# Kernel optimization log

Measured on AMD Instinct MI355X. Metric: run time of the kernel, lower is better.

Reference implementation:

```python
import jax, jax.numpy as jnp
import numpy as np

B, L, D, U = 4, 1024, 64, 32

def setup_inputs() -> dict:
    key = jax.random.key(0)
    ks = jax.random.split(key, 6)
    inputs = jax.random.normal(ks[0], (B, L, D), dtype=jnp.float32)
    Wt = jax.random.normal(ks[1], (D, U), dtype=jnp.float32) * 0.1
    Wx = jax.random.normal(ks[2], (D, U), dtype=jnp.float32) * 0.1
    Wa = jax.random.normal(ks[3], (U, 1), dtype=jnp.float32) * 0.1
    bh = jax.random.normal(ks[4], (U,), dtype=jnp.float32) * 0.1
    ba = jax.random.normal(ks[5], (1,), dtype=jnp.float32) * 0.1
    return {"inputs": inputs, "Wt": Wt, "Wx": Wx, "Wa": Wa,
            "bh": bh, "ba": ba, "attention_width": 0}

def reference(inputs, Wt, Wx, Wa, bh, ba, attention_width):
    # Additive (Bahdanau) self-attention emission.
    q = inputs @ Wt                              # (B, L, U)
    k = inputs @ Wx                              # (B, L, U)
    # broadcast add -> (B, L, L, U), the dominant intermediate
    h = jnp.tanh(q[:, :, None, :] + k[:, None, :, :] + bh)
    e = jnp.squeeze(h @ Wa, axis=-1) + ba        # (B, L, L); ba broadcasts
    # NOTE: attention_width mask is dead code in the original forward -> ignored.
    # manual max-subtracted softmax with +1e-8 denominator (as in source)
    m = jnp.max(e, axis=-1, keepdims=True)
    ex = jnp.exp(e - m)
    a = ex / (jnp.sum(ex, axis=-1, keepdims=True) + 1e-8)
    v = jnp.einsum('bij,bjd->bid', a, inputs)    # (B, L, D)
    return v
```

## Files before the change

### kernel.cpp

```cpp
#include <hip/hip_runtime.h>

#define BB 4
#define LL 1024
#define DD 64
#define UU 32
#define TI 8
#define NT 512

__global__ __launch_bounds__(256) void precompute_kernel(
    const float* __restrict__ inp, const float* __restrict__ Wt,
    const float* __restrict__ Wx, const float* __restrict__ bh,
    float* __restrict__ Eq, float* __restrict__ Ekt)
{
    __shared__ float s_in[8][DD];
    __shared__ float s_wt[DD][UU];
    __shared__ float s_wx[DD][UU];
    __shared__ float s_ek[8][36];
    int t = threadIdx.x;
    int row0 = blockIdx.x * 8;
    if (t < 128)
        ((float4*)s_in)[t] = ((const float4*)(inp + (size_t)row0 * DD))[t];
#pragma unroll
    for (int p = 0; p < 2; ++p) {
        ((float4*)s_wt)[p * 256 + t] = ((const float4*)Wt)[p * 256 + t];
        ((float4*)s_wx)[p * 256 + t] = ((const float4*)Wx)[p * 256 + t];
    }
    __syncthreads();
    int r = t >> 5;
    int u = t & 31;
    size_t row = row0 + r;
    float q = 0.f, k = 0.f;
#pragma unroll
    for (int d = 0; d < DD; ++d) {
        float x = s_in[r][d];
        q = fmaf(x, s_wt[d][u], q);
        k = fmaf(x, s_wx[d][u], k);
    }
    Eq[row * UU + u] = __expf(2.f * (q + bh[u]));
    s_ek[r][u] = __expf(2.f * k);
    __syncthreads();
    if (t < 64) {
        int u4 = t >> 3, r2 = t & 7;
        float4 v = *(const float4*)(&s_ek[r2][u4 * 4]);
        size_t gr = row0 + r2;
        size_t bb_ = gr >> 10, l = gr & 1023;
        ((float4*)Ekt)[(bb_ * 8 + u4) * LL + l] = v;
    }
}

union ShMem {
    struct { float a0[LL][4]; float a1[LL][4]; } a;
    float4 v[8][TI][16];
};

__global__ __launch_bounds__(NT) void attn_kernel(
    const float* __restrict__ Eq, const float* __restrict__ Ekt,
    const float* __restrict__ inp, const float* __restrict__ Wa,
    float* __restrict__ out)
{
    __shared__ ShMem sh;
    __shared__ float s_red[2][8][TI];

    int t  = threadIdx.x;
    int w  = t >> 6;
    int b  = blockIdx.x >> 7;
    int i0 = (blockIdx.x & 127) * TI;

    const float4* ektb = (const float4*)Ekt + (size_t)b * 8 * LL;
    const float*  eqb  = Eq + ((size_t)(b * LL + i0)) * UU;

    float acc[TI][2];
#pragma unroll
    for (int i = 0; i < TI; ++i) { acc[i][0] = 0.f; acc[i][1] = 0.f; }

    float4 cur0 = ektb[t], cur1 = ektb[NT + t];

#pragma unroll
    for (int u4 = 0; u4 < 8; ++u4) {
        float4 nxt0, nxt1;
        if (u4 < 7) {
            nxt0 = ektb[(u4 + 1) * LL + t];
            nxt1 = ektb[(u4 + 1) * LL + NT + t];
        }
        const float* waq = Wa + u4 * 4;
        float wa0 = waq[0], wa1 = waq[1], wa2 = waq[2], wa3 = waq[3];
#pragma unroll
        for (int i = 0; i < TI; ++i) {
            const float* eqq = eqb + i * UU + u4 * 4;
            float eq0 = eqq[0], eq1 = eqq[1], eq2 = eqq[2], eq3 = eqq[3];
#pragma unroll
            for (int jj = 0; jj < 2; ++jj) {
                float4 ek = jj ? cur1 : cur0;
                float p  = fmaf(eq0, ek.x, 1.f);
                float q  = fmaf(eq1, ek.y, 1.f);
                float r  = fmaf(eq2, ek.z, 1.f);
                float s  = fmaf(eq3, ek.w, 1.f);
                float n01 = fmaf(wa0, q, wa1 * p);
                float n23 = fmaf(wa2, s, wa3 * r);
                float pq = p * q, rs = r * s;
                float num = fmaf(n01, rs, n23 * pq);
                float den = pq * rs;
                acc[i][jj] = fmaf(num, __builtin_amdgcn_rcpf(den), acc[i][jj]);
            }
        }
        if (u4 < 7) { cur0 = nxt0; cur1 = nxt1; }
    }

    float ev[TI][2];
#pragma unroll
    for (int i = 0; i < TI; ++i) {
        ev[i][0] = -2.f * acc[i][0];
        ev[i][1] = -2.f * acc[i][1];
    }

    float wred[TI];
#pragma unroll
    for (int i = 0; i < TI; ++i) {
        float v = fmaxf(ev[i][0], ev[i][1]);
#pragma unroll
        for (int m = 32; m >= 1; m >>= 1) v = fmaxf(v, __shfl_xor(v, m, 64));
        wred[i] = v;
    }
    if ((t & 63) == 0) {
#pragma unroll
        for (int i = 0; i < TI; ++i) s_red[0][w][i] = wred[i];
    }
    __syncthreads();
    float m[TI];
#pragma unroll
    for (int i = 0; i < TI; ++i) {
        float v = s_red[0][0][i];
#pragma unroll
        for (int w2 = 1; w2 < 8; ++w2) v = fmaxf(v, s_red[0][w2][i]);
        m[i] = v;
    }

#pragma unroll
    for (int i = 0; i < TI; ++i) {
        ev[i][0] = __expf(ev[i][0] - m[i]);
        ev[i][1] = __expf(ev[i][1] - m[i]);
        float s = ev[i][0] + ev[i][1];
#pragma unroll
        for (int mm = 32; mm >= 1; mm >>= 1) s += __shfl_xor(s, mm, 64);
        wred[i] = s;
    }
    if ((t & 63) == 0) {
#pragma unroll
        for (int i = 0; i < TI; ++i) s_red[1][w][i] = wred[i];
    }
    __syncthreads();
    float rs[TI];
#pragma unroll
    for (int i = 0; i < TI; ++i) {
        float s = 0.f;
#pragma unroll
        for (int w2 = 0; w2 < 8; ++w2) s += s_red[1][w2][i];
        rs[i] = 1.0f / (s + 1e-8f);
    }

#pragma unroll
    for (int jj = 0; jj < 2; ++jj) {
        int j = jj * NT + t;
        float4 lo, hi;
        lo.x = ev[0][jj] * rs[0]; lo.y = ev[1][jj] * rs[1];
        lo.z = ev[2][jj] * rs[2]; lo.w = ev[3][jj] * rs[3];
        hi.x = ev[4][jj] * rs[4]; hi.y = ev[5][jj] * rs[5];
        hi.z = ev[6][jj] * rs[6]; hi.w = ev[7][jj] * rs[7];
        *(float4*)(&sh.a.a0[j][0]) = lo;
        *(float4*)(&sh.a.a1[j][0]) = hi;
    }
    __syncthreads();

    int dq = t & 15;
    int g  = t >> 4;
    const float4* inp4 = (const float4*)(inp + (size_t)b * LL * DD);
    float4 v[TI];
#pragma unroll
    for (int i = 0; i < TI; ++i) v[i] = (float4){0.f, 0.f, 0.f, 0.f};

#pragma unroll 4
    for (int jj = 0; jj < 32; ++jj) {
        int j = jj * 32 + g;
        float4 x  = inp4[j * 16 + dq];
        float4 a0 = *(const float4*)(&sh.a.a0[j][0]);
        float4 a1 = *(const float4*)(&sh.a.a1[j][0]);
        v[0].x = fmaf(a0.x, x.x, v[0].x); v[0].y = fmaf(a0.x, x.y, v[0].y);
        v[0].z = fmaf(a0.x, x.z, v[0].z); v[0].w = fmaf(a0.x, x.w, v[0].w);
        v[1].x = fmaf(a0.y, x.x, v[1].x); v[1].y = fmaf(a0.y, x.y, v[1].y);
        v[1].z = fmaf(a0.y, x.z, v[1].z); v[1].w = fmaf(a0.y, x.w, v[1].w);
        v[2].x = fmaf(a0.z, x.x, v[2].x); v[2].y = fmaf(a0.z, x.y, v[2].y);
        v[2].z = fmaf(a0.z, x.z, v[2].z); v[2].w = fmaf(a0.z, x.w, v[2].w);
        v[3].x = fmaf(a0.w, x.x, v[3].x); v[3].y = fmaf(a0.w, x.y, v[3].y);
        v[3].z = fmaf(a0.w, x.z, v[3].z); v[3].w = fmaf(a0.w, x.w, v[3].w);
        v[4].x = fmaf(a1.x, x.x, v[4].x); v[4].y = fmaf(a1.x, x.y, v[4].y);
        v[4].z = fmaf(a1.x, x.z, v[4].z); v[4].w = fmaf(a1.x, x.w, v[4].w);
        v[5].x = fmaf(a1.y, x.x, v[5].x); v[5].y = fmaf(a1.y, x.y, v[5].y);
        v[5].z = fmaf(a1.y, x.z, v[5].z); v[5].w = fmaf(a1.y, x.w, v[5].w);
        v[6].x = fmaf(a1.z, x.x, v[6].x); v[6].y = fmaf(a1.z, x.y, v[6].y);
        v[6].z = fmaf(a1.z, x.z, v[6].z); v[6].w = fmaf(a1.z, x.w, v[6].w);
        v[7].x = fmaf(a1.w, x.x, v[7].x); v[7].y = fmaf(a1.w, x.y, v[7].y);
        v[7].z = fmaf(a1.w, x.z, v[7].z); v[7].w = fmaf(a1.w, x.w, v[7].w);
    }

#pragma unroll
    for (int i = 0; i < TI; ++i) {
        v[i].x += __shfl_xor(v[i].x, 16, 64); v[i].y += __shfl_xor(v[i].y, 16, 64);
        v[i].z += __shfl_xor(v[i].z, 16, 64); v[i].w += __shfl_xor(v[i].w, 16, 64);
        v[i].x += __shfl_xor(v[i].x, 32, 64); v[i].y += __shfl_xor(v[i].y, 32, 64);
        v[i].z += __shfl_xor(v[i].z, 32, 64); v[i].w += __shfl_xor(v[i].w, 32, 64);
    }
    __syncthreads();
    if ((t & 63) < 16) {
#pragma unroll
        for (int i = 0; i < TI; ++i) sh.v[w][i][dq] = v[i];
    }
    __syncthreads();

    int i = t >> 6;
    int d = t & 63;
    const float* svf = (const float*)sh.v;
    float r = 0.f;
#pragma unroll
    for (int w2 = 0; w2 < 8; ++w2) r += svf[w2 * (TI * 64) + i * 64 + d];
    out[((size_t)b * LL + (i0 + i)) * DD + d] = r;
}

extern "C" void kernel_launch(void* const* d_in, const int* in_sizes, int n_in,
                              void* d_out, int out_size, void* d_ws, size_t ws_size,
                              hipStream_t stream) {
    const float* inp = (const float*)d_in[0];
    const float* Wt  = (const float*)d_in[1];
    const float* Wx  = (const float*)d_in[2];
    const float* Wa  = (const float*)d_in[3];
    const float* bh  = (const float*)d_in[4];
    float* out = (float*)d_out;

    float* Eq  = (float*)d_ws;
    float* Ekt = Eq + (size_t)BB * LL * UU;

    precompute_kernel<<<BB * LL / 8, 256, 0, stream>>>(inp, Wt, Wx, bh, Eq, Ekt);
    attn_kernel<<<BB * LL / TI, NT, 0, stream>>>(Eq, Ekt, inp, Wa, out);
}
```

Measured before the change: 98.20 us.

## Fuse query projection into attention kernel and prefetch input rows

```diff
diff --git a/kernel.cpp b/kernel.cpp
--- a/kernel.cpp
+++ b/kernel.cpp
@@ -8,12 +8,10 @@
 #define NT 512
 
 __global__ __launch_bounds__(256) void precompute_kernel(
-    const float* __restrict__ inp, const float* __restrict__ Wt,
-    const float* __restrict__ Wx, const float* __restrict__ bh,
-    float* __restrict__ Eq, float* __restrict__ Ekt)
+    const float* __restrict__ inp, const float* __restrict__ Wx,
+    float* __restrict__ Ekt)
 {
     __shared__ float s_in[8][DD];
-    __shared__ float s_wt[DD][UU];
     __shared__ float s_wx[DD][UU];
     __shared__ float s_ek[8][36];
     int t = threadIdx.x;
@@ -21,22 +19,15 @@
     if (t < 128)
         ((float4*)s_in)[t] = ((const float4*)(inp + (size_t)row0 * DD))[t];
 #pragma unroll
-    for (int p = 0; p < 2; ++p) {
-        ((float4*)s_wt)[p * 256 + t] = ((const float4*)Wt)[p * 256 + t];
+    for (int p = 0; p < 2; ++p)
         ((float4*)s_wx)[p * 256 + t] = ((const float4*)Wx)[p * 256 + t];
-    }
     __syncthreads();
     int r = t >> 5;
     int u = t & 31;
-    size_t row = row0 + r;
-    float q = 0.f, k = 0.f;
-#pragma unroll
-    for (int d = 0; d < DD; ++d) {
-        float x = s_in[r][d];
-        q = fmaf(x, s_wt[d][u], q);
-        k = fmaf(x, s_wx[d][u], k);
-    }
-    Eq[row * UU + u] = __expf(2.f * (q + bh[u]));
+    float k = 0.f;
+#pragma unroll
+    for (int d = 0; d < DD; ++d)
+        k = fmaf(s_in[r][d], s_wx[d][u], k);
     s_ek[r][u] = __expf(2.f * k);
     __syncthreads();
     if (t < 64) {
@@ -49,16 +40,18 @@
 }
 
 union ShMem {
+    struct { float wt[DD][UU]; float in[TI][DD]; } pre;
     struct { float a0[LL][4]; float a1[LL][4]; } a;
     float4 v[8][TI][16];
 };
 
-__global__ __launch_bounds__(NT) void attn_kernel(
-    const float* __restrict__ Eq, const float* __restrict__ Ekt,
-    const float* __restrict__ inp, const float* __restrict__ Wa,
-    float* __restrict__ out)
+__global__ __launch_bounds__(NT, 4) void attn_kernel(
+    const float* __restrict__ Ekt, const float* __restrict__ inp,
+    const float* __restrict__ Wt, const float* __restrict__ Wa,
+    const float* __restrict__ bh, float* __restrict__ out)
 {
     __shared__ ShMem sh;
+    __shared__ float s_eq[TI][UU];
     __shared__ float s_red[2][8][TI];
 
     int t  = threadIdx.x;
@@ -66,9 +59,22 @@
     int b  = blockIdx.x >> 7;
     int i0 = (blockIdx.x & 127) * TI;
 
+    if (t < 128)
+        ((float4*)sh.pre.in)[t] =
+            ((const float4*)(inp + (size_t)(b * LL + i0) * DD))[t];
+    ((float4*)sh.pre.wt)[t] = ((const float4*)Wt)[t];
+    __syncthreads();
+    if (t < TI * UU) {
+        int i = t >> 5, u = t & 31;
+        float q = 0.f;
+#pragma unroll
+        for (int d = 0; d < DD; ++d)
+            q = fmaf(sh.pre.in[i][d], sh.pre.wt[d][u], q);
+        s_eq[i][u] = __expf(2.f * (q + bh[u]));
+    }
+    __syncthreads();
+
     const float4* ektb = (const float4*)Ekt + (size_t)b * 8 * LL;
-    const float*  eqb  = Eq + ((size_t)(b * LL + i0)) * UU;
-
     float acc[TI][2];
 #pragma unroll
     for (int i = 0; i < TI; ++i) { acc[i][0] = 0.f; acc[i][1] = 0.f; }
@@ -82,12 +88,12 @@
             nxt0 = ektb[(u4 + 1) * LL + t];
             nxt1 = ektb[(u4 + 1) * LL + NT + t];
         }
-        const float* waq = Wa + u4 * 4;
-        float wa0 = waq[0], wa1 = waq[1], wa2 = waq[2], wa3 = waq[3];
+        float4 wav = *(const float4*)(Wa + u4 * 4);
+        float wa0 = wav.x, wa1 = wav.y, wa2 = wav.z, wa3 = wav.w;
 #pragma unroll
         for (int i = 0; i < TI; ++i) {
-            const float* eqq = eqb + i * UU + u4 * 4;
-            float eq0 = eqq[0], eq1 = eqq[1], eq2 = eqq[2], eq3 = eqq[3];
+            float4 eqv = *(const float4*)(&s_eq[i][u4 * 4]);
+            float eq0 = eqv.x, eq1 = eqv.y, eq2 = eqv.z, eq3 = eqv.w;
 #pragma unroll
             for (int jj = 0; jj < 2; ++jj) {
                 float4 ek = jj ? cur1 : cur0;
@@ -178,28 +184,37 @@
 #pragma unroll
     for (int i = 0; i < TI; ++i) v[i] = (float4){0.f, 0.f, 0.f, 0.f};
 
-#pragma unroll 4
-    for (int jj = 0; jj < 32; ++jj) {
-        int j = jj * 32 + g;
-        float4 x  = inp4[j * 16 + dq];
-        float4 a0 = *(const float4*)(&sh.a.a0[j][0]);
-        float4 a1 = *(const float4*)(&sh.a.a1[j][0]);
-        v[0].x = fmaf(a0.x, x.x, v[0].x); v[0].y = fmaf(a0.x, x.y, v[0].y);
-        v[0].z = fmaf(a0.x, x.z, v[0].z); v[0].w = fmaf(a0.x, x.w, v[0].w);
-        v[1].x = fmaf(a0.y, x.x, v[1].x); v[1].y = fmaf(a0.y, x.y, v[1].y);
-        v[1].z = fmaf(a0.y, x.z, v[1].z); v[1].w = fmaf(a0.y, x.w, v[1].w);
-        v[2].x = fmaf(a0.z, x.x, v[2].x); v[2].y = fmaf(a0.z, x.y, v[2].y);
-        v[2].z = fmaf(a0.z, x.z, v[2].z); v[2].w = fmaf(a0.z, x.w, v[2].w);
-        v[3].x = fmaf(a0.w, x.x, v[3].x); v[3].y = fmaf(a0.w, x.y, v[3].y);
-        v[3].z = fmaf(a0.w, x.z, v[3].z); v[3].w = fmaf(a0.w, x.w, v[3].w);
-        v[4].x = fmaf(a1.x, x.x, v[4].x); v[4].y = fmaf(a1.x, x.y, v[4].y);
-        v[4].z = fmaf(a1.x, x.z, v[4].z); v[4].w = fmaf(a1.x, x.w, v[4].w);
-        v[5].x = fmaf(a1.y, x.x, v[5].x); v[5].y = fmaf(a1.y, x.y, v[5].y);
-        v[5].z = fmaf(a1.y, x.z, v[5].z); v[5].w = fmaf(a1.y, x.w, v[5].w);
-        v[6].x = fmaf(a1.z, x.x, v[6].x); v[6].y = fmaf(a1.z, x.y, v[6].y);
-        v[6].z = fmaf(a1.z, x.z, v[6].z); v[6].w = fmaf(a1.z, x.w, v[6].w);
-        v[7].x = fmaf(a1.w, x.x, v[7].x); v[7].y = fmaf(a1.w, x.y, v[7].y);
-        v[7].z = fmaf(a1.w, x.z, v[7].z); v[7].w = fmaf(a1.w, x.w, v[7].w);
+    float4 xbuf[4];
+#pragma unroll
+    for (int p = 0; p < 4; ++p) xbuf[p] = inp4[(p * 32 + g) * 16 + dq];
+
+#pragma unroll 2
+    for (int jo = 0; jo < 8; ++jo) {
+#pragma unroll
+        for (int p = 0; p < 4; ++p) {
+            int jj = jo * 4 + p;
+            int j  = jj * 32 + g;
+            float4 x = xbuf[p];
+            if (jo < 7) xbuf[p] = inp4[((jj + 4) * 32 + g) * 16 + dq];
+            float4 a0 = *(const float4*)(&sh.a.a0[j][0]);
+            float4 a1 = *(const float4*)(&sh.a.a1[j][0]);
+            v[0].x = fmaf(a0.x, x.x, v[0].x); v[0].y = fmaf(a0.x, x.y, v[0].y);
+            v[0].z = fmaf(a0.x, x.z, v[0].z); v[0].w = fmaf(a0.x, x.w, v[0].w);
+            v[1].x = fmaf(a0.y, x.x, v[1].x); v[1].y = fmaf(a0.y, x.y, v[1].y);
+            v[1].z = fmaf(a0.y, x.z, v[1].z); v[1].w = fmaf(a0.y, x.w, v[1].w);
+            v[2].x = fmaf(a0.z, x.x, v[2].x); v[2].y = fmaf(a0.z, x.y, v[2].y);
+            v[2].z = fmaf(a0.z, x.z, v[2].z); v[2].w = fmaf(a0.z, x.w, v[2].w);
+            v[3].x = fmaf(a0.w, x.x, v[3].x); v[3].y = fmaf(a0.w, x.y, v[3].y);
+            v[3].z = fmaf(a0.w, x.z, v[3].z); v[3].w = fmaf(a0.w, x.w, v[3].w);
+            v[4].x = fmaf(a1.x, x.x, v[4].x); v[4].y = fmaf(a1.x, x.y, v[4].y);
+            v[4].z = fmaf(a1.x, x.z, v[4].z); v[4].w = fmaf(a1.x, x.w, v[4].w);
+            v[5].x = fmaf(a1.y, x.x, v[5].x); v[5].y = fmaf(a1.y, x.y, v[5].y);
+            v[5].z = fmaf(a1.y, x.z, v[5].z); v[5].w = fmaf(a1.y, x.w, v[5].w);
+            v[6].x = fmaf(a1.z, x.x, v[6].x); v[6].y = fmaf(a1.z, x.y, v[6].y);
+            v[6].z = fmaf(a1.z, x.z, v[6].z); v[6].w = fmaf(a1.z, x.w, v[6].w);
+            v[7].x = fmaf(a1.w, x.x, v[7].x); v[7].y = fmaf(a1.w, x.y, v[7].y);
+            v[7].z = fmaf(a1.w, x.z, v[7].z); v[7].w = fmaf(a1.w, x.w, v[7].w);
+        }
     }
 
 #pragma unroll
@@ -235,9 +250,8 @@
     const float* bh  = (const float*)d_in[4];
     float* out = (float*)d_out;
 
-    float* Eq  = (float*)d_ws;
-    float* Ekt = Eq + (size_t)BB * LL * UU;
-
-    precompute_kernel<<<BB * LL / 8, 256, 0, stream>>>(inp, Wt, Wx, bh, Eq, Ekt);
-    attn_kernel<<<BB * LL / TI, NT, 0, stream>>>(Eq, Ekt, inp, Wa, out);
+    float* Ekt = (float*)d_ws;
+
+    precompute_kernel<<<BB * LL / 8, 256, 0, stream>>>(inp, Wx, Ekt);
+    attn_kernel<<<BB * LL / TI, NT, 0, stream>>>(Ekt, inp, Wt, Wa, bh, out);
 }
```

Result: slower. 113.5 us (+15.6%).
